# Kernel optimization log

Measured on AMD Instinct MI355X. Metric: run time of the kernel, lower is better.

Reference implementation:

```python
import jax, jax.numpy as jnp
import numpy as np

B, C, H, W_ = 4, 256, 64, 64
INTER = 128

def conv1x1(x, w, b):
    # x: [B,C,H,W], w: [O,C], b: [O] -> [B,O,H,W]
    return jnp.einsum('bchw,oc->bohw', x, w) + b[None, :, None, None]

def setup_inputs() -> dict:
    key = jax.random.key(0)
    ks = jax.random.split(key, 5)
    s_in = 1.0 / np.sqrt(C)
    s_mid = 1.0 / np.sqrt(INTER)
    return {
        'x': jax.random.normal(ks[0], (B, C, H, W_), dtype=jnp.float32),
        'w_g': jax.random.normal(ks[1], (INTER, C), dtype=jnp.float32) * s_in,
        'b_g': jnp.zeros((INTER,), dtype=jnp.float32),
        'w_theta': jax.random.normal(ks[2], (INTER, C), dtype=jnp.float32) * s_in,
        'b_theta': jnp.zeros((INTER,), dtype=jnp.float32),
        'w_phi': jax.random.normal(ks[3], (INTER, C), dtype=jnp.float32) * s_in,
        'b_phi': jnp.zeros((INTER,), dtype=jnp.float32),
        'w_out': jax.random.normal(ks[4], (C, INTER), dtype=jnp.float32) * s_mid,
        'b_out': jnp.zeros((C,), dtype=jnp.float32),
    }

def reference(x, w_g, b_g, w_theta, b_theta, w_phi, b_phi, w_out, b_out):
    b, c, h, w = x.shape
    n = h * w
    # 1x1 conv projections, flatten spatial dims to N tokens
    g_x = conv1x1(x, w_g, b_g).reshape(b, INTER, n).transpose(0, 2, 1)      # [B,N,I]
    theta_x = conv1x1(x, w_theta, b_theta).reshape(b, INTER, n).transpose(0, 2, 1)  # [B,N,I]
    phi_x = conv1x1(x, w_phi, b_phi).reshape(b, INTER, n)                   # [B,I,N]
    f = jnp.einsum('bni,bim->bnm', theta_x, phi_x)                          # [B,N,N]
    f_div_C = jax.nn.softmax(f, axis=-1)
    y = jnp.einsum('bnm,bmi->bni', f_div_C, g_x)                            # [B,N,I]
    y = y.transpose(0, 2, 1).reshape(b, INTER, h, w)
    W_y = conv1x1(y, w_out, b_out)                                          # [B,C,H,W]
    return W_y + x
```

## Files before the change

### kernel.cpp

```cpp
#include <hip/hip_runtime.h>

#define BB 4
#define CC 256
#define NN 4096
#define II 128
#define NSPLIT 4
#define KVH (NN / NSPLIT)
#define NT (KVH / 64)
#define LOG2E 1.4426950408889634f

typedef float f32x4 __attribute__((ext_vector_type(4)));
typedef _Float16 f16x8 __attribute__((ext_vector_type(8)));

static __device__ __forceinline__ unsigned short f2h(float f) {
    _Float16 h = (_Float16)f;
    return __builtin_bit_cast(unsigned short, h);
}
static __device__ __forceinline__ float h2f(unsigned short s) {
    return (float)__builtin_bit_cast(_Float16, s);
}
static __device__ __forceinline__ unsigned int pack2h(float a, float b) {
    return (unsigned int)f2h(a) | ((unsigned int)f2h(b) << 16);
}

__global__ void conv_wout_kernel(const float* __restrict__ w, unsigned short* __restrict__ o) {
    int i = blockIdx.x * 256 + threadIdx.x;
    o[i] = f2h(w[i]);
}

__global__ __launch_bounds__(256) void proj_kernel(
    const float* __restrict__ x,
    const float* __restrict__ w_th, const float* __restrict__ b_th,
    const float* __restrict__ w_ph, const float* __restrict__ b_ph,
    const float* __restrict__ w_g,  const float* __restrict__ b_g,
    unsigned short* __restrict__ Qb, unsigned short* __restrict__ Kb,
    unsigned short* __restrict__ Vt)
{
    __shared__ char lds[24576];
    unsigned short* wl = (unsigned short*)lds;
    unsigned short* xl = (unsigned short*)(lds + 16384);

    int tid = threadIdx.x;
    int w = tid >> 6, l = tid & 63, g = l >> 4, cl = l & 15;
    int mat = blockIdx.z, b = blockIdx.y, n0 = blockIdx.x * 64;
    const float* wp = (mat == 0) ? w_th : (mat == 1) ? w_ph : w_g;
    const float* bp = (mat == 0) ? b_th : (mat == 1) ? b_ph : b_g;

    f32x4 acc[2][4];
    #pragma unroll
    for (int it = 0; it < 2; ++it)
        #pragma unroll
        for (int nt = 0; nt < 4; ++nt) acc[it][nt] = (f32x4){0.f, 0.f, 0.f, 0.f};

    const float* xb = x + (size_t)b * CC * NN;
    int c2 = tid >> 3, nch = tid & 7;

    for (int c0 = 0; c0 < CC; c0 += 64) {
        __syncthreads();
        #pragma unroll
        for (int r = 0; r < 4; ++r) {
            int idx = r * 256 + tid;
            int row = idx >> 3, ch = idx & 7;
            const float* src = wp + row * CC + c0 + ch * 8;
            float4 a = *(const float4*)src;
            float4 bq = *(const float4*)(src + 4);
            union { unsigned short s[8]; uint4 q; } pk;
            pk.s[0] = f2h(a.x); pk.s[1] = f2h(a.y); pk.s[2] = f2h(a.z); pk.s[3] = f2h(a.w);
            pk.s[4] = f2h(bq.x); pk.s[5] = f2h(bq.y); pk.s[6] = f2h(bq.z); pk.s[7] = f2h(bq.w);
            *(uint4*)((char*)wl + row * 128 + ((ch ^ (row & 7)) << 4)) = pk.q;
        }
        {
            const float* xsrc = xb + (size_t)(c0 + c2 * 2) * NN + n0 + nch * 8;
            float4 x00 = *(const float4*)xsrc;
            float4 x01 = *(const float4*)(xsrc + 4);
            float4 x10 = *(const float4*)(xsrc + NN);
            float4 x11 = *(const float4*)(xsrc + NN + 4);
            float lo[8] = {x00.x, x00.y, x00.z, x00.w, x01.x, x01.y, x01.z, x01.w};
            float hi[8] = {x10.x, x10.y, x10.z, x10.w, x11.x, x11.y, x11.z, x11.w};
            #pragma unroll
            for (int t = 0; t < 8; ++t) {
                int n = nch * 8 + t;
                *(unsigned int*)((char*)xl + n * 128 + ((c2 * 4) ^ ((n & 7) << 4))) = pack2h(lo[t], hi[t]);
            }
        }
        __syncthreads();
        #pragma unroll
        for (int kc = 0; kc < 2; ++kc) {
            f16x8 af[2], bf[4];
            #pragma unroll
            for (int it = 0; it < 2; ++it) {
                int row = w * 32 + it * 16 + cl;
                af[it] = *(const f16x8*)((const char*)wl + row * 128 + (((kc * 4 + g) ^ (row & 7)) << 4));
            }
            #pragma unroll
            for (int nt = 0; nt < 4; ++nt) {
                int row = nt * 16 + cl;
                bf[nt] = *(const f16x8*)((const char*)xl + row * 128 + (((kc * 4 + g) ^ (row & 7)) << 4));
            }
            #pragma unroll
            for (int it = 0; it < 2; ++it)
                #pragma unroll
                for (int nt = 0; nt < 4; ++nt)
                    acc[it][nt] = __builtin_amdgcn_mfma_f32_16x16x32_f16(af[it], bf[nt], acc[it][nt], 0, 0, 0);
        }
    }

    float bv[2][4];
    #pragma unroll
    for (int it = 0; it < 2; ++it)
        #pragma unroll
        for (int r = 0; r < 4; ++r) bv[it][r] = bp[w * 32 + it * 16 + 4 * g + r];
    float scale = (mat == 0) ? LOG2E : 1.0f;

    __syncthreads();
    if (mat < 2) {
        unsigned short* pk = (unsigned short*)lds;
        #pragma unroll
        for (int it = 0; it < 2; ++it)
            #pragma unroll
            for (int nt = 0; nt < 4; ++nt)
                #pragma unroll
                for (int r = 0; r < 4; r += 2) {
                    int n = nt * 16 + cl;
                    int i = w * 32 + it * 16 + 4 * g + r;
                    unsigned int v = pack2h((acc[it][nt][r] + bv[it][r]) * scale,
                                            (acc[it][nt][r + 1] + bv[it][r + 1]) * scale);
                    *(unsigned int*)((char*)pk + n * 256 + ((i * 2) ^ ((n & 7) << 4))) = v;
                }
        __syncthreads();
        unsigned short* out = (mat == 0) ? Qb : Kb;
        #pragma unroll
        for (int r = 0; r < 4; ++r) {
            int idx = r * 256 + tid;
            int n = idx >> 4, seg = idx & 15;
            uint4 q = *(const uint4*)((const char*)pk + n * 256 + ((seg << 4) ^ ((n & 7) << 4)));
            *(uint4*)(out + (size_t)(b * NN + n0 + n) * II + seg * 8) = q;
        }
    } else {
        unsigned short* pk = (unsigned short*)lds;
        #pragma unroll
        for (int it = 0; it < 2; ++it)
            #pragma unroll
            for (int nt = 0; nt < 4; ++nt)
                #pragma unroll
                for (int r = 0; r < 4; ++r) {
                    int i = w * 32 + it * 16 + 4 * g + r;
                    int n = nt * 16 + cl;
                    *(unsigned short*)((char*)pk + i * 128 + ((n * 2) ^ ((i & 7) << 4))) =
                        f2h(acc[it][nt][r] + bv[it][r]);
                }
        __syncthreads();
        #pragma unroll
        for (int r = 0; r < 4; ++r) {
            int idx = r * 256 + tid;
            int i = idx >> 3, seg = idx & 7;
            uint4 q = *(const uint4*)((const char*)pk + i * 128 + ((seg << 4) ^ ((i & 7) << 4)));
            *(uint4*)(Vt + (size_t)(b * II + i) * NN + n0 + seg * 8) = q;
        }
    }
}

__global__ __launch_bounds__(256, 2) void attn_kernel(
    const unsigned short* __restrict__ Qb,
    const unsigned short* __restrict__ Kb,
    const unsigned short* __restrict__ Vb,
    unsigned short* __restrict__ Yp,
    float2* __restrict__ ML)
{
    __shared__ unsigned short Ks[64 * 128];
    __shared__ unsigned short Vs[128 * 64];

    int tid = threadIdx.x;
    int w = tid >> 6, l = tid & 63, g = l >> 4, cl = l & 15;
    int id = blockIdx.x;
    int comb = (id & 7) * 2 + ((id >> 3) & 1);
    int b = comb >> 2, sp = comb & 3, qt = id >> 4;
    int qr0 = qt * 128;
    int m_base = sp * KVH;

    f16x8 qa0[4], qa1[4];
    {
        const unsigned short* qrow0 = Qb + (size_t)(b * NN + qr0 + w * 32 + cl) * II;
        const unsigned short* qrow1 = qrow0 + 16 * II;
        #pragma unroll
        for (int kc = 0; kc < 4; ++kc) {
            qa0[kc] = *(const f16x8*)(qrow0 + kc * 32 + g * 8);
            qa1[kc] = *(const f16x8*)(qrow1 + kc * 32 + g * 8);
        }
    }

    f32x4 yacc0[8], yacc1[8];
    #pragma unroll
    for (int it = 0; it < 8; ++it) {
        yacc0[it] = (f32x4){0.f, 0.f, 0.f, 0.f};
        yacc1[it] = (f32x4){0.f, 0.f, 0.f, 0.f};
    }
    float mrun0 = -1e30f, lrun0 = 0.f, mrun1 = -1e30f, lrun1 = 0.f;

    const unsigned short* kb = Kb + (size_t)(b * NN + m_base) * II;
    const unsigned short* vb = Vb + (size_t)b * II * NN + m_base;
    int krow = tid >> 4, kch = tid & 15;
    int vrow = tid >> 3, vch = tid & 7;
    int kswz = (kch ^ (krow & 7)) << 4;
    int vsw = (vrow & 7) << 4;
    int vc0 = ((vch >> 2) * 32 + (vch & 1) * 16 + ((vch >> 1) & 1) * 4) * 2;

    uint4 k0, k1, k2, k3, v0, v1, v2, v3;
    k0 = *(const uint4*)(kb + (size_t)(krow) * II + kch * 8);
    k1 = *(const uint4*)(kb + (size_t)(16 + krow) * II + kch * 8);
    k2 = *(const uint4*)(kb + (size_t)(32 + krow) * II + kch * 8);
    k3 = *(const uint4*)(kb + (size_t)(48 + krow) * II + kch * 8);
    v0 = *(const uint4*)(vb + (size_t)(vrow) * NN + vch * 8);
    v1 = *(const uint4*)(vb + (size_t)(32 + vrow) * NN + vch * 8);
    v2 = *(const uint4*)(vb + (size_t)(64 + vrow) * NN + vch * 8);
    v3 = *(const uint4*)(vb + (size_t)(96 + vrow) * NN + vch * 8);

    for (int t = 0; t < NT; ++t) {
        __syncthreads();
        *(uint4*)((char*)Ks + (krow) * 256 + kswz) = k0;
        *(uint4*)((char*)Ks + (16 + krow) * 256 + kswz) = k1;
        *(uint4*)((char*)Ks + (32 + krow) * 256 + kswz) = k2;
        *(uint4*)((char*)Ks + (48 + krow) * 256 + kswz) = k3;
        {
            uint2 lo, hi;
            lo.x = v0.x; lo.y = v0.y; hi.x = v0.z; hi.y = v0.w;
            *(uint2*)((char*)Vs + (vrow) * 128 + (vc0 ^ vsw)) = lo;
            *(uint2*)((char*)Vs + (vrow) * 128 + ((vc0 + 16) ^ vsw)) = hi;
            lo.x = v1.x; lo.y = v1.y; hi.x = v1.z; hi.y = v1.w;
            *(uint2*)((char*)Vs + (32 + vrow) * 128 + (vc0 ^ vsw)) = lo;
            *(uint2*)((char*)Vs + (32 + vrow) * 128 + ((vc0 + 16) ^ vsw)) = hi;
            lo.x = v2.x; lo.y = v2.y; hi.x = v2.z; hi.y = v2.w;
            *(uint2*)((char*)Vs + (64 + vrow) * 128 + (vc0 ^ vsw)) = lo;
            *(uint2*)((char*)Vs + (64 + vrow) * 128 + ((vc0 + 16) ^ vsw)) = hi;
            lo.x = v3.x; lo.y = v3.y; hi.x = v3.z; hi.y = v3.w;
            *(uint2*)((char*)Vs + (96 + vrow) * 128 + (vc0 ^ vsw)) = lo;
            *(uint2*)((char*)Vs + (96 + vrow) * 128 + ((vc0 + 16) ^ vsw)) = hi;
        }
        __syncthreads();
        if (t + 1 < NT) {
            const unsigned short* kp = kb + (size_t)(t + 1) * 64 * II;
            k0 = *(const uint4*)(kp + (size_t)(krow) * II + kch * 8);
            k1 = *(const uint4*)(kp + (size_t)(16 + krow) * II + kch * 8);
            k2 = *(const uint4*)(kp + (size_t)(32 + krow) * II + kch * 8);
            k3 = *(const uint4*)(kp + (size_t)(48 + krow) * II + kch * 8);
        }

        f32x4 s0[4], s1[4];
        #pragma unroll
        for (int mt = 0; mt < 4; ++mt) {
            s0[mt] = (f32x4){0.f, 0.f, 0.f, 0.f};
            s1[mt] = (f32x4){0.f, 0.f, 0.f, 0.f};
        }
        __builtin_amdgcn_s_setprio(1);
        #pragma unroll
        for (int mt = 0; mt < 4; ++mt) {
            int row = mt * 16 + cl;
            #pragma unroll
            for (int kc = 0; kc < 4; ++kc) {
                f16x8 kf = *(const f16x8*)((const char*)Ks + row * 256 + (((kc * 4 + g) ^ (row & 7)) << 4));
                s0[mt] = __builtin_amdgcn_mfma_f32_16x16x32_f16(kf, qa0[kc], s0[mt], 0, 0, 0);
                s1[mt] = __builtin_amdgcn_mfma_f32_16x16x32_f16(kf, qa1[kc], s1[mt], 0, 0, 0);
            }
        }
        __builtin_amdgcn_s_setprio(0);
        if (t + 1 < NT) {
            const unsigned short* vp = vb + (size_t)(t + 1) * 64;
            v0 = *(const uint4*)(vp + (size_t)(vrow) * NN + vch * 8);
            v1 = *(const uint4*)(vp + (size_t)(32 + vrow) * NN + vch * 8);
            v2 = *(const uint4*)(vp + (size_t)(64 + vrow) * NN + vch * 8);
            v3 = *(const uint4*)(vp + (size_t)(96 + vrow) * NN + vch * 8);
        }

        union { _Float16 h[8]; f16x8 v; } pb00, pb01, pb10, pb11;
        {
            float tmax = fmaxf(fmaxf(fmaxf(s0[0][0], s0[0][1]), fmaxf(s0[0][2], s0[0][3])),
                               fmaxf(fmaxf(s0[1][0], s0[1][1]), fmaxf(s0[1][2], s0[1][3])));
            tmax = fmaxf(tmax, fmaxf(fmaxf(fmaxf(s0[2][0], s0[2][1]), fmaxf(s0[2][2], s0[2][3])),
                                     fmaxf(fmaxf(s0[3][0], s0[3][1]), fmaxf(s0[3][2], s0[3][3]))));
            tmax = fmaxf(tmax, __shfl_xor(tmax, 16));
            tmax = fmaxf(tmax, __shfl_xor(tmax, 32));
            if (!__all(tmax <= mrun0 + 8.0f)) {
                float mnew = fmaxf(mrun0, tmax);
                float corr = exp2f(mrun0 - mnew);
                mrun0 = mnew;
                lrun0 *= corr;
                #pragma unroll
                for (int it = 0; it < 8; ++it)
                    #pragma unroll
                    for (int r = 0; r < 4; ++r) yacc0[it][r] *= corr;
            }
            float ps = 0.f;
            #pragma unroll
            for (int j = 0; j < 8; ++j) {
                float p0 = exp2f(s0[j >> 2][j & 3] - mrun0);
                float p1 = exp2f(s0[2 + (j >> 2)][j & 3] - mrun0);
                _Float16 h0 = (_Float16)p0, h1 = (_Float16)p1;
                ps += (float)h0 + (float)h1;
                pb00.h[j] = h0; pb01.h[j] = h1;
            }
            ps += __shfl_xor(ps, 16);
            ps += __shfl_xor(ps, 32);
            lrun0 += ps;
        }
        {
            float tmax = fmaxf(fmaxf(fmaxf(s1[0][0], s1[0][1]), fmaxf(s1[0][2], s1[0][3])),
                               fmaxf(fmaxf(s1[1][0], s1[1][1]), fmaxf(s1[1][2], s1[1][3])));
            tmax = fmaxf(tmax, fmaxf(fmaxf(fmaxf(s1[2][0], s1[2][1]), fmaxf(s1[2][2], s1[2][3])),
                                     fmaxf(fmaxf(s1[3][0], s1[3][1]), fmaxf(s1[3][2], s1[3][3]))));
            tmax = fmaxf(tmax, __shfl_xor(tmax, 16));
            tmax = fmaxf(tmax, __shfl_xor(tmax, 32));
            if (!__all(tmax <= mrun1 + 8.0f)) {
                float mnew = fmaxf(mrun1, tmax);
                float corr = exp2f(mrun1 - mnew);
                mrun1 = mnew;
                lrun1 *= corr;
                #pragma unroll
                for (int it = 0; it < 8; ++it)
                    #pragma unroll
                    for (int r = 0; r < 4; ++r) yacc1[it][r] *= corr;
            }
            float ps = 0.f;
            #pragma unroll
            for (int j = 0; j < 8; ++j) {
                float p0 = exp2f(s1[j >> 2][j & 3] - mrun1);
                float p1 = exp2f(s1[2 + (j >> 2)][j & 3] - mrun1);
                _Float16 h0 = (_Float16)p0, h1 = (_Float16)p1;
                ps += (float)h0 + (float)h1;
                pb10.h[j] = h0; pb11.h[j] = h1;
            }
            ps += __shfl_xor(ps, 16);
            ps += __shfl_xor(ps, 32);
            lrun1 += ps;
        }

        __builtin_amdgcn_s_setprio(1);
        #pragma unroll
        for (int it = 0; it < 8; ++it) {
            int row = it * 16 + cl;
            f16x8 vf0 = *(const f16x8*)((const char*)Vs + row * 128 + ((g ^ (row & 7)) << 4));
            f16x8 vf1 = *(const f16x8*)((const char*)Vs + row * 128 + (((4 + g) ^ (row & 7)) << 4));
            yacc0[it] = __builtin_amdgcn_mfma_f32_16x16x32_f16(vf0, pb00.v, yacc0[it], 0, 0, 0);
            yacc0[it] = __builtin_amdgcn_mfma_f32_16x16x32_f16(vf1, pb01.v, yacc0[it], 0, 0, 0);
            yacc1[it] = __builtin_amdgcn_mfma_f32_16x16x32_f16(vf0, pb10.v, yacc1[it], 0, 0, 0);
            yacc1[it] = __builtin_amdgcn_mfma_f32_16x16x32_f16(vf1, pb11.v, yacc1[it], 0, 0, 0);
        }
        __builtin_amdgcn_s_setprio(0);
    }

    __syncthreads();

    unsigned short* ys = Ks + w * 2048;
    size_t rowbase0 = (size_t)((sp * BB + b) * NN + qr0 + w * 32);
    int prow = l >> 2;
    {
        float rl = 1.0f / lrun0;
        #pragma unroll
        for (int it = 0; it < 8; ++it)
            #pragma unroll
            for (int r = 0; r < 4; r += 2) {
                int i = it * 16 + 4 * g + r;
                *(unsigned int*)((char*)ys + cl * 256 + ((i * 2) ^ ((cl & 7) << 4))) =
                    pack2h(yacc0[it][r] * rl, yacc0[it][r + 1] * rl);
            }
        #pragma unroll
        for (int c = 0; c < 4; ++c) {
            int seg = c * 4 + (l & 3);
            uint4 q = *(const uint4*)((const char*)ys + prow * 256 + ((seg << 4) ^ ((prow & 7) << 4)));
            *(uint4*)(Yp + (rowbase0 + prow) * II + seg * 8) = q;
        }
    }
    {
        float rl = 1.0f / lrun1;
        #pragma unroll
        for (int it = 0; it < 8; ++it)
            #pragma unroll
            for (int r = 0; r < 4; r += 2) {
                int i = it * 16 + 4 * g + r;
                *(unsigned int*)((char*)ys + cl * 256 + ((i * 2) ^ ((cl & 7) << 4))) =
                    pack2h(yacc1[it][r] * rl, yacc1[it][r + 1] * rl);
            }
        #pragma unroll
        for (int c = 0; c < 4; ++c) {
            int seg = c * 4 + (l & 3);
            uint4 q = *(const uint4*)((const char*)ys + prow * 256 + ((seg << 4) ^ ((prow & 7) << 4)));
            *(uint4*)(Yp + (rowbase0 + 16 + prow) * II + seg * 8) = q;
        }
    }
    if (l < 16) {
        float2 v; v.x = mrun0; v.y = lrun0;
        ML[rowbase0 + l] = v;
    } else if (l < 32) {
        float2 v; v.x = mrun1; v.y = lrun1;
        ML[rowbase0 + 16 + (l - 16)] = v;
    }
}

__global__ __launch_bounds__(256) void combine_kernel(
    const unsigned short* __restrict__ Yp, const float2* __restrict__ ML,
    const unsigned short* __restrict__ Wo, const float* __restrict__ b_out,
    const float* __restrict__ x, float* __restrict__ out)
{
    __shared__ unsigned short Ys[4][16 * 128];

    int tid = threadIdx.x;
    int w = tid >> 6, l = tid & 63, g = l >> 4, cl = l & 15;
    int qt = blockIdx.x, b = blockIdx.y;
    int qr0 = qt * 64;
    int n = qr0 + w * 16 + cl;

    float ms[NSPLIT], ls[NSPLIT], wgt[NSPLIT];
    float M = -1e30f;
    #pragma unroll
    for (int s = 0; s < NSPLIT; ++s) {
        float2 ml = ML[(size_t)(s * BB + b) * NN + n];
        ms[s] = ml.x; ls[s] = ml.y;
        M = fmaxf(M, ml.x);
    }
    float wsum = 0.f;
    #pragma unroll
    for (int s = 0; s < NSPLIT; ++s) { wgt[s] = exp2f(ms[s] - M) * ls[s]; wsum += wgt[s]; }
    float rd = 1.0f / wsum;
    #pragma unroll
    for (int s = 0; s < NSPLIT; ++s) wgt[s] *= rd;

    unsigned short* ys = Ys[w];
    #pragma unroll
    for (int j = 0; j < 4; ++j) {
        float acc[8];
        #pragma unroll
        for (int e = 0; e < 8; ++e) acc[e] = 0.f;
        #pragma unroll
        for (int s = 0; s < NSPLIT; ++s) {
            union { unsigned short s16[8]; uint4 q; } a;
            a.q = *(const uint4*)(Yp + ((size_t)(s * BB + b) * NN + n) * II + g * 32 + j * 8);
            #pragma unroll
            for (int e = 0; e < 8; ++e) acc[e] += wgt[s] * h2f(a.s16[e]);
        }
        union { unsigned short s16[8]; uint4 q; } o;
        #pragma unroll
        for (int e = 0; e < 8; ++e) o.s16[e] = f2h(acc[e]);
        *(uint4*)((char*)ys + cl * 256 + (((g * 4 + j) ^ (cl & 7)) << 4)) = o.q;
    }

    f32x4 zero4 = {0.f, 0.f, 0.f, 0.f};
    f16x8 yf[4];
    #pragma unroll
    for (int kc = 0; kc < 4; ++kc)
        yf[kc] = *(const f16x8*)((const char*)ys + cl * 256 + (((kc * 4 + g) ^ (cl & 7)) << 4));
    for (int ct = 0; ct < 16; ++ct) {
        f32x4 oa = zero4;
        #pragma unroll
        for (int kc = 0; kc < 4; ++kc) {
            f16x8 wf = *(const f16x8*)(Wo + (ct * 16 + cl) * II + kc * 32 + g * 8);
            oa = __builtin_amdgcn_mfma_f32_16x16x32_f16(wf, yf[kc], oa, 0, 0, 0);
        }
        #pragma unroll
        for (int r = 0; r < 4; ++r) {
            int c = ct * 16 + 4 * g + r;
            size_t off = (size_t)(b * CC + c) * NN + n;
            out[off] = oa[r] + b_out[c] + x[off];
        }
    }
}

extern "C" void kernel_launch(void* const* d_in, const int* in_sizes, int n_in,
                              void* d_out, int out_size, void* d_ws, size_t ws_size,
                              hipStream_t stream) {
    const float* x     = (const float*)d_in[0];
    const float* w_g   = (const float*)d_in[1];
    const float* b_g   = (const float*)d_in[2];
    const float* w_th  = (const float*)d_in[3];
    const float* b_th  = (const float*)d_in[4];
    const float* w_ph  = (const float*)d_in[5];
    const float* b_ph  = (const float*)d_in[6];
    const float* w_out = (const float*)d_in[7];
    const float* b_o   = (const float*)d_in[8];
    float* out = (float*)d_out;

    const size_t SZ = (size_t)BB * NN * II;
    unsigned short* Qb = (unsigned short*)d_ws;
    unsigned short* Kb = Qb + SZ;
    unsigned short* Vt = Kb + SZ;
    unsigned short* Wo = Vt + SZ;
    unsigned short* Yp = Wo + (size_t)CC * II;
    float2*         ML = (float2*)(Yp + (size_t)NSPLIT * SZ);

    conv_wout_kernel<<<dim3((CC * II) / 256), dim3(256), 0, stream>>>(w_out, Wo);
    proj_kernel<<<dim3(NN / 64, BB, 3), dim3(256), 0, stream>>>(
        x, w_th, b_th, w_ph, b_ph, w_g, b_g, Qb, Kb, Vt);
    attn_kernel<<<dim3(NSPLIT * BB * (NN / 128)), dim3(256), 0, stream>>>(
        Qb, Kb, Vt, Yp, ML);
    combine_kernel<<<dim3(NN / 64, BB), dim3(256), 0, stream>>>(Yp, ML, Wo, b_o, x, out);
}
```

Baseline: 109.2 us.

## Fold w_out conversion into proj, compute softmax row sums via MFMA

Removes the separate w_out fp16 conversion launch by having block x==0 of the V-projection path write the converted Wo inside proj_kernel. In the attention kernel, the per-row probability sums are now accumulated with an MFMA against a ones vector instead of scalar adds and cross-lane shuffles. The exp results are packed with the round-toward-zero pack intrinsic, and the max reduction uses three-input max groupings. This trades one launch and some VALU/shuffle work for extra MFMA instructions and slight rounding differences in the sums.

```diff
diff --git a/kernel.cpp b/kernel.cpp
--- a/kernel.cpp
+++ b/kernel.cpp
@@ -22,19 +22,19 @@
 static __device__ __forceinline__ unsigned int pack2h(float a, float b) {
     return (unsigned int)f2h(a) | ((unsigned int)f2h(b) << 16);
 }
-
-__global__ void conv_wout_kernel(const float* __restrict__ w, unsigned short* __restrict__ o) {
-    int i = blockIdx.x * 256 + threadIdx.x;
-    o[i] = f2h(w[i]);
-}
+static __device__ __forceinline__ unsigned int cvt2h(float a, float b) {
+    return __builtin_bit_cast(unsigned int, __builtin_amdgcn_cvt_pkrtz(a, b));
+}
+#define M3(a, b, c) fmaxf(fmaxf((a), (b)), (c))
 
 __global__ __launch_bounds__(256) void proj_kernel(
     const float* __restrict__ x,
     const float* __restrict__ w_th, const float* __restrict__ b_th,
     const float* __restrict__ w_ph, const float* __restrict__ b_ph,
     const float* __restrict__ w_g,  const float* __restrict__ b_g,
+    const float* __restrict__ w_out,
     unsigned short* __restrict__ Qb, unsigned short* __restrict__ Kb,
-    unsigned short* __restrict__ Vt)
+    unsigned short* __restrict__ Vt, unsigned short* __restrict__ Wo)
 {
     __shared__ char lds[24576];
     unsigned short* wl = (unsigned short*)lds;
@@ -64,9 +64,9 @@
             const float* src = wp + row * CC + c0 + ch * 8;
             float4 a = *(const float4*)src;
             float4 bq = *(const float4*)(src + 4);
-            union { unsigned short s[8]; uint4 q; } pk;
-            pk.s[0] = f2h(a.x); pk.s[1] = f2h(a.y); pk.s[2] = f2h(a.z); pk.s[3] = f2h(a.w);
-            pk.s[4] = f2h(bq.x); pk.s[5] = f2h(bq.y); pk.s[6] = f2h(bq.z); pk.s[7] = f2h(bq.w);
+            union { unsigned int u[4]; uint4 q; } pk;
+            pk.u[0] = pack2h(a.x, a.y);  pk.u[1] = pack2h(a.z, a.w);
+            pk.u[2] = pack2h(bq.x, bq.y); pk.u[3] = pack2h(bq.z, bq.w);
             *(uint4*)((char*)wl + row * 128 + ((ch ^ (row & 7)) << 4)) = pk.q;
         }
         {
@@ -157,6 +157,18 @@
             uint4 q = *(const uint4*)((const char*)pk + i * 128 + ((seg << 4) ^ ((i & 7) << 4)));
             *(uint4*)(Vt + (size_t)(b * II + i) * NN + n0 + seg * 8) = q;
         }
+        if (blockIdx.x == 0) {
+            #pragma unroll
+            for (int r = 0; r < 16; ++r) {
+                int idx = (r * 256 + tid) * 8;
+                float4 a = *(const float4*)(w_out + idx);
+                float4 b4 = *(const float4*)(w_out + idx + 4);
+                union { unsigned int u[4]; uint4 q; } pw;
+                pw.u[0] = pack2h(a.x, a.y);   pw.u[1] = pack2h(a.z, a.w);
+                pw.u[2] = pack2h(b4.x, b4.y); pw.u[3] = pack2h(b4.z, b4.w);
+                *(uint4*)&Wo[idx] = pw.q;
+            }
+        }
     }
 }
 
@@ -188,14 +200,18 @@
             qa1[kc] = *(const f16x8*)(qrow1 + kc * 32 + g * 8);
         }
     }
-
-    f32x4 yacc0[8], yacc1[8];
+    const f16x8 onesv = {(_Float16)1.f, (_Float16)1.f, (_Float16)1.f, (_Float16)1.f,
+                         (_Float16)1.f, (_Float16)1.f, (_Float16)1.f, (_Float16)1.f};
+
+    f32x4 yacc0[8], yacc1[8], lacc0, lacc1;
     #pragma unroll
     for (int it = 0; it < 8; ++it) {
         yacc0[it] = (f32x4){0.f, 0.f, 0.f, 0.f};
         yacc1[it] = (f32x4){0.f, 0.f, 0.f, 0.f};
     }
-    float mrun0 = -1e30f, lrun0 = 0.f, mrun1 = -1e30f, lrun1 = 0.f;
+    lacc0 = (f32x4){0.f, 0.f, 0.f, 0.f};
+    lacc1 = (f32x4){0.f, 0.f, 0.f, 0.f};
+    float mrun0 = -1e30f, mrun1 = -1e30f;
 
     const unsigned short* kb = Kb + (size_t)(b * NN + m_base) * II;
     const unsigned short* vb = Vb + (size_t)b * II * NN + m_base;
@@ -271,69 +287,69 @@
             v3 = *(const uint4*)(vp + (size_t)(96 + vrow) * NN + vch * 8);
         }
 
-        union { _Float16 h[8]; f16x8 v; } pb00, pb01, pb10, pb11;
+        union { unsigned int u[4]; f16x8 v; } pb00, pb01, pb10, pb11;
         {
-            float tmax = fmaxf(fmaxf(fmaxf(s0[0][0], s0[0][1]), fmaxf(s0[0][2], s0[0][3])),
-                               fmaxf(fmaxf(s0[1][0], s0[1][1]), fmaxf(s0[1][2], s0[1][3])));
-            tmax = fmaxf(tmax, fmaxf(fmaxf(fmaxf(s0[2][0], s0[2][1]), fmaxf(s0[2][2], s0[2][3])),
-                                     fmaxf(fmaxf(s0[3][0], s0[3][1]), fmaxf(s0[3][2], s0[3][3]))));
+            float t0 = M3(s0[0][0], s0[0][1], s0[0][2]);
+            float t1 = M3(s0[0][3], s0[1][0], s0[1][1]);
+            float t2 = M3(s0[1][2], s0[1][3], s0[2][0]);
+            float t3 = M3(s0[2][1], s0[2][2], s0[2][3]);
+            float t4 = M3(s0[3][0], s0[3][1], s0[3][2]);
+            float tmax = fmaxf(M3(t0, t1, t2), M3(t3, t4, s0[3][3]));
             tmax = fmaxf(tmax, __shfl_xor(tmax, 16));
             tmax = fmaxf(tmax, __shfl_xor(tmax, 32));
             if (!__all(tmax <= mrun0 + 8.0f)) {
                 float mnew = fmaxf(mrun0, tmax);
                 float corr = exp2f(mrun0 - mnew);
                 mrun0 = mnew;
-                lrun0 *= corr;
                 #pragma unroll
                 for (int it = 0; it < 8; ++it)
                     #pragma unroll
                     for (int r = 0; r < 4; ++r) yacc0[it][r] *= corr;
-            }
-            float ps = 0.f;
-            #pragma unroll
-            for (int j = 0; j < 8; ++j) {
-                float p0 = exp2f(s0[j >> 2][j & 3] - mrun0);
-                float p1 = exp2f(s0[2 + (j >> 2)][j & 3] - mrun0);
-                _Float16 h0 = (_Float16)p0, h1 = (_Float16)p1;
-                ps += (float)h0 + (float)h1;
-                pb00.h[j] = h0; pb01.h[j] = h1;
-            }
-            ps += __shfl_xor(ps, 16);
-            ps += __shfl_xor(ps, 32);
-            lrun0 += ps;
+                #pragma unroll
+                for (int r = 0; r < 4; ++r) lacc0[r] *= corr;
+            }
+            #pragma unroll
+            for (int mt = 0; mt < 4; ++mt) {
+                unsigned int ua = cvt2h(exp2f(s0[mt][0] - mrun0), exp2f(s0[mt][1] - mrun0));
+                unsigned int ub = cvt2h(exp2f(s0[mt][2] - mrun0), exp2f(s0[mt][3] - mrun0));
+                if (mt < 2) { pb00.u[mt * 2] = ua; pb00.u[mt * 2 + 1] = ub; }
+                else        { pb01.u[(mt - 2) * 2] = ua; pb01.u[(mt - 2) * 2 + 1] = ub; }
+            }
         }
         {
-            float tmax = fmaxf(fmaxf(fmaxf(s1[0][0], s1[0][1]), fmaxf(s1[0][2], s1[0][3])),
-                               fmaxf(fmaxf(s1[1][0], s1[1][1]), fmaxf(s1[1][2], s1[1][3])));
-            tmax = fmaxf(tmax, fmaxf(fmaxf(fmaxf(s1[2][0], s1[2][1]), fmaxf(s1[2][2], s1[2][3])),
-                                     fmaxf(fmaxf(s1[3][0], s1[3][1]), fmaxf(s1[3][2], s1[3][3]))));
+            float t0 = M3(s1[0][0], s1[0][1], s1[0][2]);
+            float t1 = M3(s1[0][3], s1[1][0], s1[1][1]);
+            float t2 = M3(s1[1][2], s1[1][3], s1[2][0]);
+            float t3 = M3(s1[2][1], s1[2][2], s1[2][3]);
+            float t4 = M3(s1[3][0], s1[3][1], s1[3][2]);
+            float tmax = fmaxf(M3(t0, t1, t2), M3(t3, t4, s1[3][3]));
             tmax = fmaxf(tmax, __shfl_xor(tmax, 16));
             tmax = fmaxf(tmax, __shfl_xor(tmax, 32));
             if (!__all(tmax <= mrun1 + 8.0f)) {
                 float mnew = fmaxf(mrun1, tmax);
                 float corr = exp2f(mrun1 - mnew);
                 mrun1 = mnew;
-                lrun1 *= corr;
                 #pragma unroll
                 for (int it = 0; it < 8; ++it)
                     #pragma unroll
                     for (int r = 0; r < 4; ++r) yacc1[it][r] *= corr;
-            }
-            float ps = 0.f;
-            #pragma unroll
-            for (int j = 0; j < 8; ++j) {
-                float p0 = exp2f(s1[j >> 2][j & 3] - mrun1);
-                float p1 = exp2f(s1[2 + (j >> 2)][j & 3] - mrun1);
-                _Float16 h0 = (_Float16)p0, h1 = (_Float16)p1;
-                ps += (float)h0 + (float)h1;
-                pb10.h[j] = h0; pb11.h[j] = h1;
-            }
-            ps += __shfl_xor(ps, 16);
-            ps += __shfl_xor(ps, 32);
-            lrun1 += ps;
+                #pragma unroll
+                for (int r = 0; r < 4; ++r) lacc1[r] *= corr;
+            }
+            #pragma unroll
+            for (int mt = 0; mt < 4; ++mt) {
+                unsigned int ua = cvt2h(exp2f(s1[mt][0] - mrun1), exp2f(s1[mt][1] - mrun1));
+                unsigned int ub = cvt2h(exp2f(s1[mt][2] - mrun1), exp2f(s1[mt][3] - mrun1));
+                if (mt < 2) { pb10.u[mt * 2] = ua; pb10.u[mt * 2 + 1] = ub; }
+                else        { pb11.u[(mt - 2) * 2] = ua; pb11.u[(mt - 2) * 2 + 1] = ub; }
+            }
         }
 
         __builtin_amdgcn_s_setprio(1);
+        lacc0 = __builtin_amdgcn_mfma_f32_16x16x32_f16(onesv, pb00.v, lacc0, 0, 0, 0);
+        lacc0 = __builtin_amdgcn_mfma_f32_16x16x32_f16(onesv, pb01.v, lacc0, 0, 0, 0);
+        lacc1 = __builtin_amdgcn_mfma_f32_16x16x32_f16(onesv, pb10.v, lacc1, 0, 0, 0);
+        lacc1 = __builtin_amdgcn_mfma_f32_16x16x32_f16(onesv, pb11.v, lacc1, 0, 0, 0);
         #pragma unroll
         for (int it = 0; it < 8; ++it) {
             int row = it * 16 + cl;
@@ -353,7 +369,7 @@
     size_t rowbase0 = (size_t)((sp * BB + b) * NN + qr0 + w * 32);
     int prow = l >> 2;
     {
-        float rl = 1.0f / lrun0;
+        float rl = 1.0f / lacc0[0];
         #pragma unroll
         for (int it = 0; it < 8; ++it)
             #pragma unroll
@@ -370,7 +386,7 @@
         }
     }
     {
-        float rl = 1.0f / lrun1;
+        float rl = 1.0f / lacc1[0];
         #pragma unroll
         for (int it = 0; it < 8; ++it)
             #pragma unroll
@@ -387,10 +403,10 @@
         }
     }
     if (l < 16) {
-        float2 v; v.x = mrun0; v.y = lrun0;
+        float2 v; v.x = mrun0; v.y = lacc0[0];
         ML[rowbase0 + l] = v;
     } else if (l < 32) {
-        float2 v; v.x = mrun1; v.y = lrun1;
+        float2 v; v.x = mrun1; v.y = lacc1[0];
         ML[rowbase0 + 16 + (l - 16)] = v;
     }
 }
@@ -436,9 +452,9 @@
             #pragma unroll
             for (int e = 0; e < 8; ++e) acc[e] += wgt[s] * h2f(a.s16[e]);
         }
-        union { unsigned short s16[8]; uint4 q; } o;
-        #pragma unroll
-        for (int e = 0; e < 8; ++e) o.s16[e] = f2h(acc[e]);
+        union { unsigned int u[4]; uint4 q; } o;
+        #pragma unroll
+        for (int e = 0; e < 4; ++e) o.u[e] = pack2h(acc[e * 2], acc[e * 2 + 1]);
         *(uint4*)((char*)ys + cl * 256 + (((g * 4 + j) ^ (cl & 7)) << 4)) = o.q;
     }
 
@@ -485,9 +501,8 @@
     unsigned short* Yp = Wo + (size_t)CC * II;
     float2*         ML = (float2*)(Yp + (size_t)NSPLIT * SZ);
 
-    conv_wout_kernel<<<dim3((CC * II) / 256), dim3(256), 0, stream>>>(w_out, Wo);
     proj_kernel<<<dim3(NN / 64, BB, 3), dim3(256), 0, stream>>>(
-        x, w_th, b_th, w_ph, b_ph, w_g, b_g, Qb, Kb, Vt);
+        x, w_th, b_th, w_ph, b_ph, w_g, b_g, w_out, Qb, Kb, Vt, Wo);
     attn_kernel<<<dim3(NSPLIT * BB * (NN / 128)), dim3(256), 0, stream>>>(
         Qb, Kb, Vt, Yp, ML);
     combine_kernel<<<dim3(NN / 64, BB), dim3(256), 0, stream>>>(Yp, ML, Wo, b_o, x, out);
```

Result: faster. 99.80 us (-8.6%).
